# Performance work log

Hardware: AMD Instinct MI355X
Metric: run time of the kernel (lower is better)

The kernel has to match this reference:

```python
import jax, jax.numpy as jnp
import numpy as np

B, N = 4096, 8192
RETURN_W, SHARPE_W, CONC_W, CONF_W, BENT_W, AUX_W = 1.0, 0.1, 0.01, 0.1, 0.01, 0.1
RETURN_TEMP = 20.0
NEG = -1e30
EPS = 1e-8


def setup_inputs() -> dict:
    key = jax.random.key(0)
    ks = jax.random.split(key, 6)
    portfolio_returns = jax.random.normal(ks[0], (B,), dtype=jnp.float32) * 0.01
    weights = jax.random.uniform(ks[1], (B, N), dtype=jnp.float32)
    confidence = jax.random.uniform(ks[2], (B, N), dtype=jnp.float32)
    actual_returns = jax.random.normal(ks[3], (B, N), dtype=jnp.float32) * 0.02
    masks = (jax.random.uniform(ks[4], (B, N)) > 0.1).astype(jnp.float32)
    scores = jax.random.normal(ks[5], (B, N), dtype=jnp.float32)
    return {
        "portfolio_returns": portfolio_returns,
        "weights": weights,
        "confidence": confidence,
        "actual_returns": actual_returns,
        "masks": masks,
        "scores": scores,
    }


def _ranking_loss(scores, returns, masks):
    # Vectorized ListNet loss: masked softmax over valid stocks per sample.
    valid = masks > 0  # (B, N) bool
    n_valid = valid.sum(axis=-1)  # (B,)
    target = jax.nn.softmax(jnp.where(valid, returns * RETURN_TEMP, NEG), axis=-1)
    log_dist = jax.nn.log_softmax(jnp.where(valid, scores, NEG), axis=-1)
    per_sample = -(target * jnp.where(valid, log_dist, 0.0)).sum(axis=-1)
    per_sample = per_sample / jnp.maximum(n_valid, 1).astype(per_sample.dtype)
    sample_ok = n_valid >= 2  # (B,) samples with >=2 valid stocks
    num_ok = sample_ok.sum()
    total = jnp.where(sample_ok, per_sample, 0.0).sum()
    return jnp.where(num_ok > 0, total / jnp.maximum(num_ok, 1), 0.0)


def reference(portfolio_returns, weights, confidence, actual_returns, masks, scores):
    # return maximization
    mean_return = portfolio_returns.mean()
    return_loss = -mean_return
    # sharpe (batch_size > 1; torch .std() uses ddof=1)
    return_std = jnp.std(portfolio_returns, ddof=1)
    sharpe_loss = jnp.clip(-mean_return / (return_std + 0.01), -10.0, 10.0)
    # concentration (weight entropy)
    concentration_loss = -(weights * jnp.log(weights + EPS)).sum(axis=-1).mean()
    # confidence loss
    selected_conf = (weights * confidence * masks).sum(axis=-1)
    total_weight = (weights * masks).sum(axis=-1) + EPS
    per_sample_conf = selected_conf / total_weight
    conf_targets = jax.nn.sigmoid(portfolio_returns * 50.0)
    confidence_loss = jnp.mean((per_sample_conf - conf_targets) ** 2)
    # batch entropy (stocks never valid contribute exactly 0, so no index-filter needed)
    normalized_weights = weights / (weights.sum(axis=-1, keepdims=True) + EPS)
    avg_sel = (normalized_weights * masks).mean(axis=0)  # (N,)
    avg_sel = avg_sel / (avg_sel.sum() + EPS)
    batch_entropy = -(avg_sel * jnp.log(avg_sel + EPS)).sum()
    batch_entropy_loss = -batch_entropy
    # auxiliary ranking loss
    auxiliary_loss = _ranking_loss(scores, actual_returns, masks)
    total_loss = (
        RETURN_W * return_loss
        + SHARPE_W * sharpe_loss
        + CONC_W * concentration_loss
        + CONF_W * confidence_loss
        + BENT_W * batch_entropy_loss
        + AUX_W * auxiliary_loss
    )
    return total_loss
```

## Files before the change

### kernel.cpp

```cpp
#include <hip/hip_runtime.h>
#include <math.h>

#define BB 4096
#define NN 8192
#define EPSF 1e-8f

typedef float f32x4 __attribute__((ext_vector_type(4)));
typedef unsigned short u16x4 __attribute__((ext_vector_type(4)));

#define ST2  8192
#define PPF  73728
#define SCAL 4096
#define CS   8192

__device__ __forceinline__ unsigned short f2bf(float f) {
    union { float f; unsigned u; } v; v.f = f;
    unsigned u = v.u + 0x7FFF + ((v.u >> 16) & 1);
    return (unsigned short)(u >> 16);
}

__global__ void init_ws(float* __restrict__ ws) {
    int i = blockIdx.x * blockDim.x + threadIdx.x;
    if (i < 12288) ws[SCAL + i] = 0.f;
}

template<int MODE>
__global__ __launch_bounds__(512) void main_k(
    const float* __restrict__ pr, const float* __restrict__ w,
    const float* __restrict__ cf, const float* __restrict__ ar,
    const float* __restrict__ mk, const float* __restrict__ sc,
    float* ws)
{
    extern __shared__ f32x4 wlds[];
    __shared__ float rpark[8][2];
    __shared__ float park[2][8][8];

    const int t = threadIdx.x;
    const int wave = t >> 6, lane = t & 63;
    const int rowBase = blockIdx.x * 2;

    const size_t rbase = (size_t)rowBase * (NN / 4);
    const f32x4* w4 = (const f32x4*)w;
    const f32x4* m4 = (const f32x4*)mk;
    const f32x4* c4 = (const f32x4*)cf;
    const f32x4* a4 = (const f32x4*)ar;
    const f32x4* s4 = (const f32x4*)sc;

    float rs0, rs1;
    {
        float rsv[2];
#pragma unroll
        for (int rr = 0; rr < 2; ++rr) {
            float acc = 0.f;
#pragma unroll
            for (int j = 0; j < 4; ++j) {
                const int idx = rr * 2048 + j * 512 + t;
                const f32x4 v = __builtin_nontemporal_load(w4 + rbase + idx);
                wlds[idx] = v;
                acc += (v.x + v.y) + (v.z + v.w);
            }
            rsv[rr] = acc;
        }
        rs0 = rsv[0]; rs1 = rsv[1];
    }
#pragma unroll
    for (int off = 32; off; off >>= 1) {
        rs0 += __shfl_xor(rs0, off);
        rs1 += __shfl_xor(rs1, off);
    }
    if (lane == 0) { rpark[wave][0] = rs0; rpark[wave][1] = rs1; }
    __syncthreads();

    float inv[2];
#pragma unroll
    for (int r = 0; r < 2; ++r) {
        float acc = 0.f;
#pragma unroll
        for (int k = 0; k < 8; ++k) acc += rpark[k][r];
        inv[r] = 1.f / (acc + EPSF);
    }

    float csum[16];
#pragma unroll
    for (int j = 0; j < 16; ++j) csum[j] = 0.f;

#define PROC(WK, MKV, CK, RK, SK, IDX) {                          \
        const float wk = (WK), mval = (MKV);                      \
        conc = fmaf(wk, __logf(wk + EPSF), conc);                 \
        const float wmk = wk * mval;                              \
        tw += wmk; scf = fmaf(wmk, (CK), scf);                    \
        nv += mval;                                               \
        const float er = __expf((RK) * 20.f) * mval;              \
        Zr += er; A = fmaf(er, (SK), A);                          \
        Zs = fmaf(__expf((SK)), mval, Zs);                        \
        csum[IDX] = fmaf(wmk, invr, csum[IDX]); }

#pragma unroll
    for (int rr = 0; rr < 2; ++rr) {
        const size_t base = rbase + (size_t)rr * (NN / 4) + t;
        const float invr = inv[rr];
        float conc = 0.f, scf = 0.f, tw = 0.f, nv = 0.f;
        float Zr = 0.f, A = 0.f, Zs = 0.f;
#pragma unroll
        for (int j = 0; j < 4; ++j) {
            const f32x4 wv = wlds[rr * 2048 + j * 512 + t];
            const f32x4 mv = __builtin_nontemporal_load(m4 + base + j * 512);
            const f32x4 cv = __builtin_nontemporal_load(c4 + base + j * 512);
            const f32x4 rv = __builtin_nontemporal_load(a4 + base + j * 512);
            const f32x4 sv = __builtin_nontemporal_load(s4 + base + j * 512);
            PROC(wv.x, mv.x, cv.x, rv.x, sv.x, j * 4 + 0)
            PROC(wv.y, mv.y, cv.y, rv.y, sv.y, j * 4 + 1)
            PROC(wv.z, mv.z, cv.z, rv.z, sv.z, j * 4 + 2)
            PROC(wv.w, mv.w, cv.w, rv.w, sv.w, j * 4 + 3)
        }
#pragma unroll
        for (int off = 32; off; off >>= 1) {
            conc += __shfl_xor(conc, off);
            scf  += __shfl_xor(scf, off);
            tw   += __shfl_xor(tw, off);
            nv   += __shfl_xor(nv, off);
            Zr   += __shfl_xor(Zr, off);
            A    += __shfl_xor(A, off);
            Zs   += __shfl_xor(Zs, off);
        }
        if (lane == 0) {
            float* p = park[rr][wave];
            p[0] = conc; p[1] = scf; p[2] = tw; p[3] = nv;
            p[4] = Zr;   p[5] = A;   p[6] = Zs;
        }
    }
#undef PROC

    if (MODE == 1) {
        unsigned short* bfrow = (unsigned short*)(ws + PPF) + (size_t)blockIdx.x * NN;
#pragma unroll
        for (int j = 0; j < 4; ++j) {
            u16x4 v;
            v.x = f2bf(csum[j * 4 + 0]); v.y = f2bf(csum[j * 4 + 1]);
            v.z = f2bf(csum[j * 4 + 2]); v.w = f2bf(csum[j * 4 + 3]);
            __builtin_nontemporal_store(v, (u16x4*)bfrow + t + j * 512);
        }
    } else {
#pragma unroll
        for (int j = 0; j < 4; ++j) {
            const int f4 = t + j * 512;
            atomicAdd(&ws[CS + 4 * f4 + 0], csum[j * 4 + 0]);
            atomicAdd(&ws[CS + 4 * f4 + 1], csum[j * 4 + 1]);
            atomicAdd(&ws[CS + 4 * f4 + 2], csum[j * 4 + 2]);
            atomicAdd(&ws[CS + 4 * f4 + 3], csum[j * 4 + 3]);
        }
    }

    __syncthreads();

    if (t < 64) {
        float c0 = 0.f, c1 = 0.f, c2 = 0.f, c3 = 0.f;
        if (lane < 2) {
            float CO = 0, SC = 0, TW = 0, NV = 0, ZR = 0, AA = 0, ZS = 0;
#pragma unroll
            for (int k = 0; k < 8; ++k) {
                const float* p = park[lane][k];
                CO += p[0]; SC += p[1]; TW += p[2]; NV += p[3];
                ZR += p[4]; AA += p[5]; ZS += p[6];
            }
            c0 = CO;
            const float psc = SC / (TW + EPSF);
            const float ct = 1.f / (1.f + __expf(-50.f * pr[rowBase + lane]));
            const float d = psc - ct;
            c1 = d * d;
            if (NV >= 2.f) {
                c2 = (__logf(ZS) - AA / ZR) / NV;
                c3 = 1.f;
            }
        }
        c0 += __shfl_xor(c0, 1);
        c1 += __shfl_xor(c1, 1);
        c2 += __shfl_xor(c2, 1);
        c3 += __shfl_xor(c3, 1);
        if (lane == 0) {
            if (MODE == 1) {
                float* dst = ws + (size_t)blockIdx.x * 4;
                dst[0] = c0; dst[1] = c1; dst[2] = c2; dst[3] = c3;
            } else {
                atomicAdd(&ws[SCAL + 0], c0);
                atomicAdd(&ws[SCAL + 1], c1);
                atomicAdd(&ws[SCAL + 2], c2);
                atomicAdd(&ws[SCAL + 3], c3);
            }
        }
    }
}

__global__ __launch_bounds__(128) void colreduce_k(const unsigned short* __restrict__ src,
                                                   float* __restrict__ st2) {
    const int col4 = blockIdx.x * 128 + threadIdx.x;
    const int k0 = blockIdx.y * 256;
    const u16x4* s4 = (const u16x4*)src;
    float a0 = 0.f, a1 = 0.f, a2 = 0.f, a3 = 0.f;
    for (int k = 0; k < 256; ++k) {
        const u16x4 v = s4[(size_t)(k0 + k) * (NN / 4) + col4];
        union { unsigned u; float f; } b;
        b.u = (unsigned)v.x << 16; a0 += b.f;
        b.u = (unsigned)v.y << 16; a1 += b.f;
        b.u = (unsigned)v.z << 16; a2 += b.f;
        b.u = (unsigned)v.w << 16; a3 += b.f;
    }
    f32x4 o; o.x = a0; o.y = a1; o.z = a2; o.w = a3;
    *((f32x4*)(st2 + (size_t)blockIdx.y * NN) + col4) = o;
}

__device__ __forceinline__ float block_sum_1024(float v) {
    __shared__ float scm[16];
#pragma unroll
    for (int off = 32; off; off >>= 1) v += __shfl_xor(v, off);
    if ((threadIdx.x & 63) == 0) scm[threadIdx.x >> 6] = v;
    __syncthreads();
    if (threadIdx.x == 0) {
        float a = 0.f;
        for (int k = 0; k < 16; ++k) a += scm[k];
        scm[0] = a;
    }
    __syncthreads();
    float r = scm[0];
    __syncthreads();
    return r;
}

template<int MODE>
__global__ __launch_bounds__(1024) void finalize(
    const float* __restrict__ pr, const float* __restrict__ ws,
    float* __restrict__ out)
{
    __shared__ float colLDS[NN];
    const int t = threadIdx.x;

    float s = 0.f, ssq = 0.f;
    for (int i = t; i < BB; i += 1024) { float v = pr[i]; s += v; ssq = fmaf(v, v, ssq); }

    float p0 = 0.f, p1 = 0.f, p2 = 0.f, p3 = 0.f;
    if (MODE == 1) {
        for (int b = t; b < 2048; b += 1024) {
            p0 += ws[b * 4 + 0]; p1 += ws[b * 4 + 1];
            p2 += ws[b * 4 + 2]; p3 += ws[b * 4 + 3];
        }
    }

    float Tc = 0.f;
    for (int i = t; i < NN; i += 1024) {
        float cs;
        if (MODE == 1) {
            cs = 0.f;
#pragma unroll
            for (int k = 0; k < 8; ++k) cs += ws[ST2 + k * NN + i];
        } else {
            cs = ws[CS + i];
        }
        colLDS[i] = cs;
        Tc += cs;
    }

    float S  = block_sum_1024(s);
    float SS = block_sum_1024(ssq);
    float T  = block_sum_1024(Tc);
    float C0, C1, C2, C3;
    if (MODE == 1) {
        C0 = block_sum_1024(p0); C1 = block_sum_1024(p1);
        C2 = block_sum_1024(p2); C3 = block_sum_1024(p3);
    } else {
        C0 = ws[SCAL + 0]; C1 = ws[SCAL + 1];
        C2 = ws[SCAL + 2]; C3 = ws[SCAL + 3];
    }

    const float mean = S / (float)BB;
    const float denom = T / (float)BB + EPSF;

    float ent = 0.f;
    for (int i = t; i < NN; i += 1024) {
        float a = colLDS[i] / (float)BB;
        float na = a / denom;
        ent = fmaf(na, __logf(na + EPSF), ent);
    }
    float ENT = block_sum_1024(ent);

    if (t == 0) {
        float var = (SS - (float)BB * mean * mean) / (float)(BB - 1);
        float sd = sqrtf(fmaxf(var, 0.f));
        float sharpe = -mean / (sd + 0.01f);
        sharpe = fminf(fmaxf(sharpe, -10.f), 10.f);
        float conc_loss = -C0 / (float)BB;
        float conf_loss =  C1 / (float)BB;
        float aux = (C3 > 0.f) ? C2 / fmaxf(C3, 1.f) : 0.f;
        out[0] = 1.0f * (-mean)
               + 0.1f * sharpe
               + 0.01f * conc_loss
               + 0.1f * conf_loss
               + 0.01f * ENT
               + 0.1f * aux;
    }
}

extern "C" void kernel_launch(void* const* d_in, const int* in_sizes, int n_in,
                              void* d_out, int out_size, void* d_ws, size_t ws_size,
                              hipStream_t stream) {
    const float* pr = (const float*)d_in[0];
    const float* w  = (const float*)d_in[1];
    const float* cf = (const float*)d_in[2];
    const float* ar = (const float*)d_in[3];
    const float* mk = (const float*)d_in[4];
    const float* sc = (const float*)d_in[5];
    float* ws = (float*)d_ws;
    float* out = (float*)d_out;

    const size_t ldsBytes = 2 * (NN / 4) * sizeof(f32x4);
    const size_t bfNeed = (size_t)PPF * 4 + (size_t)2048 * NN * 2;

    if (ws_size >= bfNeed) {
        main_k<1><<<2048, 512, ldsBytes, stream>>>(pr, w, cf, ar, mk, sc, ws);
        colreduce_k<<<dim3(16, 8), 128, 0, stream>>>(
            (const unsigned short*)(ws + PPF), ws + ST2);
        finalize<1><<<1, 1024, 0, stream>>>(pr, ws, out);
    } else {
        init_ws<<<48, 256, 0, stream>>>(ws);
        main_k<0><<<2048, 512, ldsBytes, stream>>>(pr, w, cf, ar, mk, sc, ws);
        finalize<0><<<1, 1024, 0, stream>>>(pr, ws, out);
    }
}
```

Measured before the change: 151.3 us.

## Drop LDS staging of weights, re-read from cache; widen column reduce with atomics

The main kernel no longer stages the two weight rows (64 KB) in LDS. It re-reads them from global memory in the second pass, relying on L2/MALL hits, and adds a launch-bounds occupancy hint so more blocks fit per CU. The column reduction now uses 64 row-chunks of 32 instead of 8 of 256, accumulating into a zeroed column buffer with atomics. This removes the partial-sum layer that finalize had to read. The trade-off is a second weight read that may miss cache, plus an extra init launch and atomic contention.

```diff
diff --git a/kernel.cpp b/kernel.cpp
--- a/kernel.cpp
+++ b/kernel.cpp
@@ -8,10 +8,9 @@
 typedef float f32x4 __attribute__((ext_vector_type(4)));
 typedef unsigned short u16x4 __attribute__((ext_vector_type(4)));
 
-#define ST2  8192
-#define PPF  73728
+#define CS   8192
+#define PPF  16384
 #define SCAL 4096
-#define CS   8192
 
 __device__ __forceinline__ unsigned short f2bf(float f) {
     union { float f; unsigned u; } v; v.f = f;
@@ -19,19 +18,23 @@
     return (unsigned short)(u >> 16);
 }
 
+__global__ void initcol_k(float* __restrict__ ws) {
+    int i = blockIdx.x * blockDim.x + threadIdx.x;
+    if (i < NN) ws[CS + i] = 0.f;
+}
+
 __global__ void init_ws(float* __restrict__ ws) {
     int i = blockIdx.x * blockDim.x + threadIdx.x;
     if (i < 12288) ws[SCAL + i] = 0.f;
 }
 
 template<int MODE>
-__global__ __launch_bounds__(512) void main_k(
+__global__ __launch_bounds__(512, 8) void main_k(
     const float* __restrict__ pr, const float* __restrict__ w,
     const float* __restrict__ cf, const float* __restrict__ ar,
     const float* __restrict__ mk, const float* __restrict__ sc,
     float* ws)
 {
-    extern __shared__ f32x4 wlds[];
     __shared__ float rpark[8][2];
     __shared__ float park[2][8][8];
 
@@ -54,9 +57,7 @@
             float acc = 0.f;
 #pragma unroll
             for (int j = 0; j < 4; ++j) {
-                const int idx = rr * 2048 + j * 512 + t;
-                const f32x4 v = __builtin_nontemporal_load(w4 + rbase + idx);
-                wlds[idx] = v;
+                const f32x4 v = w4[rbase + rr * 2048 + j * 512 + t];
                 acc += (v.x + v.y) + (v.z + v.w);
             }
             rsv[rr] = acc;
@@ -103,7 +104,7 @@
         float Zr = 0.f, A = 0.f, Zs = 0.f;
 #pragma unroll
         for (int j = 0; j < 4; ++j) {
-            const f32x4 wv = wlds[rr * 2048 + j * 512 + t];
+            const f32x4 wv = w4[base + j * 512];
             const f32x4 mv = __builtin_nontemporal_load(m4 + base + j * 512);
             const f32x4 cv = __builtin_nontemporal_load(c4 + base + j * 512);
             const f32x4 rv = __builtin_nontemporal_load(a4 + base + j * 512);
@@ -192,12 +193,12 @@
 }
 
 __global__ __launch_bounds__(128) void colreduce_k(const unsigned short* __restrict__ src,
-                                                   float* __restrict__ st2) {
+                                                   float* __restrict__ ws) {
     const int col4 = blockIdx.x * 128 + threadIdx.x;
-    const int k0 = blockIdx.y * 256;
+    const int k0 = blockIdx.y * 32;
     const u16x4* s4 = (const u16x4*)src;
     float a0 = 0.f, a1 = 0.f, a2 = 0.f, a3 = 0.f;
-    for (int k = 0; k < 256; ++k) {
+    for (int k = 0; k < 32; ++k) {
         const u16x4 v = s4[(size_t)(k0 + k) * (NN / 4) + col4];
         union { unsigned u; float f; } b;
         b.u = (unsigned)v.x << 16; a0 += b.f;
@@ -205,8 +206,10 @@
         b.u = (unsigned)v.z << 16; a2 += b.f;
         b.u = (unsigned)v.w << 16; a3 += b.f;
     }
-    f32x4 o; o.x = a0; o.y = a1; o.z = a2; o.w = a3;
-    *((f32x4*)(st2 + (size_t)blockIdx.y * NN) + col4) = o;
+    atomicAdd(&ws[CS + col4 * 4 + 0], a0);
+    atomicAdd(&ws[CS + col4 * 4 + 1], a1);
+    atomicAdd(&ws[CS + col4 * 4 + 2], a2);
+    atomicAdd(&ws[CS + col4 * 4 + 3], a3);
 }
 
 __device__ __forceinline__ float block_sum_1024(float v) {
@@ -247,14 +250,7 @@
 
     float Tc = 0.f;
     for (int i = t; i < NN; i += 1024) {
-        float cs;
-        if (MODE == 1) {
-            cs = 0.f;
-#pragma unroll
-            for (int k = 0; k < 8; ++k) cs += ws[ST2 + k * NN + i];
-        } else {
-            cs = ws[CS + i];
-        }
+        float cs = ws[CS + i];
         colLDS[i] = cs;
         Tc += cs;
     }
@@ -311,17 +307,17 @@
     float* ws = (float*)d_ws;
     float* out = (float*)d_out;
 
-    const size_t ldsBytes = 2 * (NN / 4) * sizeof(f32x4);
     const size_t bfNeed = (size_t)PPF * 4 + (size_t)2048 * NN * 2;
 
     if (ws_size >= bfNeed) {
-        main_k<1><<<2048, 512, ldsBytes, stream>>>(pr, w, cf, ar, mk, sc, ws);
-        colreduce_k<<<dim3(16, 8), 128, 0, stream>>>(
-            (const unsigned short*)(ws + PPF), ws + ST2);
+        initcol_k<<<32, 256, 0, stream>>>(ws);
+        main_k<1><<<2048, 512, 0, stream>>>(pr, w, cf, ar, mk, sc, ws);
+        colreduce_k<<<dim3(16, 64), 128, 0, stream>>>(
+            (const unsigned short*)(ws + PPF), ws);
         finalize<1><<<1, 1024, 0, stream>>>(pr, ws, out);
     } else {
         init_ws<<<48, 256, 0, stream>>>(ws);
-        main_k<0><<<2048, 512, ldsBytes, stream>>>(pr, w, cf, ar, mk, sc, ws);
+        main_k<0><<<2048, 512, 0, stream>>>(pr, w, cf, ar, mk, sc, ws);
         finalize<0><<<1, 1024, 0, stream>>>(pr, ws, out);
     }
 }
```

Measured after the change: 195.8 us. 1.29x slower.
